# Optimization experiments

Measured on AMD Instinct MI355X. Metric: run time of the kernel, lower is better.

The kernel has to match this reference:

```python
import jax, jax.numpy as jnp
import numpy as np

N = 50000      # nodes
E = 800000     # edges
F_IN = 128     # num_features
H = 64         # hidden_dim
G = 64         # graphs in batch
EPS = 1e-5


def setup_inputs() -> dict:
    ks = jax.random.split(jax.random.key(0), 16)
    x = jax.random.normal(ks[0], (N, F_IN), dtype=jnp.float32)
    edge_index = jax.random.randint(ks[1], (2, E), 0, N, dtype=jnp.int64)
    batch = jnp.sort(jax.random.randint(ks[2], (N,), 0, G, dtype=jnp.int64))
    s = 0.05
    inp = {"x": x, "edge_index": edge_index, "batch": batch}
    # GCNConv layers: W [out,in], bias [out]; BatchNorm gamma/beta [H]
    dims = [(H, F_IN), (H, H), (H, H)]
    for i, (o, ci) in enumerate(dims):
        inp[f"W{i}"] = jax.random.normal(ks[3 + i], (o, ci), dtype=jnp.float32) * s
        inp[f"b{i}"] = jnp.zeros((o,), dtype=jnp.float32)
        inp[f"g{i}"] = jnp.ones((o,), dtype=jnp.float32)
        inp[f"be{i}"] = jnp.zeros((o,), dtype=jnp.float32)
    inp["lin1_w"] = jax.random.normal(ks[10], (H // 2, H), dtype=jnp.float32) * s
    inp["lin1_b"] = jnp.zeros((H // 2,), dtype=jnp.float32)
    inp["lin2_w"] = jax.random.normal(ks[11], (1, H // 2), dtype=jnp.float32) * s
    inp["lin2_b"] = jnp.zeros((1,), dtype=jnp.float32)
    return inp


def _gcn_conv(x, src, dst, W, b):
    # PyG GCNConv: h = x W^T; add self-loops; symmetric deg^{-1/2} norm; scatter-add; + bias
    h = x @ W.T                                   # [N, out]
    n = x.shape[0]
    deg = jax.ops.segment_sum(jnp.ones(src.shape[0], h.dtype), dst, num_segments=n) + 1.0
    dinv = jax.lax.rsqrt(deg)                     # [N]
    msg = h[src] * (dinv[src] * dinv[dst])[:, None]   # per-edge messages
    agg = jax.ops.segment_sum(msg, dst, num_segments=n)
    agg = agg + h * (dinv * dinv)[:, None]        # self-loop contribution
    return agg + b


def _bn_relu(x, g, be):
    # BatchNorm1d (training-mode batch stats, biased var) + ReLU; dropout = identity (eval)
    m = x.mean(axis=0)
    v = jnp.var(x, axis=0)
    return jax.nn.relu((x - m) * jax.lax.rsqrt(v + EPS) * g + be)


def reference(x, edge_index, batch,
              W0, b0, g0, be0, W1, b1, g1, be1, W2, b2, g2, be2,
              lin1_w, lin1_b, lin2_w, lin2_b):
    src, dst = edge_index[0], edge_index[1]
    Ws = [(W0, b0, g0, be0), (W1, b1, g1, be1), (W2, b2, g2, be2)]
    h = x
    for (W, b, g, be) in Ws:
        h = _bn_relu(_gcn_conv(h, src, dst, W, b), g, be)
    # global mean pool over graphs
    sums = jax.ops.segment_sum(h, batch, num_segments=G)          # [G, H]
    cnt = jax.ops.segment_sum(jnp.ones((h.shape[0],), h.dtype), batch, num_segments=G)
    pooled = sums / jnp.maximum(cnt, 1.0)[:, None]
    h = jax.nn.relu(pooled @ lin1_w.T + lin1_b)
    return h @ lin2_w.T + lin2_b                                   # [G, 1]
```

## Files before the change

### kernel.cpp

```cpp
#include <hip/hip_runtime.h>

#define NN 50000
#define NE 800000
#define FIN 128
#define H 64
#define NG 64
#define BN_EPS 1e-5f
#define INV_N (1.0f / 50000.0f)
#define NB_SCAN 196
#define NBKT 196

__global__ void deg_count(const int* __restrict__ dst, int* __restrict__ deg, int E) {
    int e = blockIdx.x * blockDim.x + threadIdx.x;
    if (e < E) atomicAdd(&deg[dst[e]], 1);
}

__global__ void setup_misc(const int* __restrict__ deg, float* __restrict__ dinv,
                           const float* __restrict__ W0, const float* __restrict__ W1,
                           const float* __restrict__ W2, float* __restrict__ Wt0,
                           float* __restrict__ Wt1, float* __restrict__ Wt2,
                           float* __restrict__ sl0, float* __restrict__ sl1,
                           float* __restrict__ sl2, float* __restrict__ poolcnt, int n) {
    int i = blockIdx.x * 256 + threadIdx.x;
    if (i < n) dinv[i] = rsqrtf((float)deg[i] + 1.0f);
    if (i < 64 * 128) { sl0[i] = 0.f; sl1[i] = 0.f; sl2[i] = 0.f; }
    if (i < NG * H + NG) poolcnt[i] = 0.f;
    if (i < FIN * 64) {
        int k = i >> 6, o = i & 63;
        Wt0[i] = W0[o * FIN + k];
    }
    if (i < H * 64) {
        int k = i >> 6, o = i & 63;
        Wt1[i] = W1[o * H + k];
        Wt2[i] = W2[o * H + k];
    }
}

__global__ void scan_block(const int* __restrict__ deg, int* __restrict__ row_start,
                           int* __restrict__ aux, int n) {
    __shared__ int s[256];
    int i = blockIdx.x * 256 + threadIdx.x;
    int v = (i < n) ? deg[i] : 0;
    s[threadIdx.x] = v;
    __syncthreads();
    for (int off = 1; off < 256; off <<= 1) {
        int t = (threadIdx.x >= off) ? s[threadIdx.x - off] : 0;
        __syncthreads();
        s[threadIdx.x] += t;
        __syncthreads();
    }
    if (i < n) row_start[i] = s[threadIdx.x] - v;
    if (threadIdx.x == 255) aux[blockIdx.x] = s[255];
}

__global__ void scan_aux(int* __restrict__ aux, int nb) {
    __shared__ int s[256];
    int v = (threadIdx.x < nb) ? aux[threadIdx.x] : 0;
    s[threadIdx.x] = v;
    __syncthreads();
    for (int off = 1; off < 256; off <<= 1) {
        int t = (threadIdx.x >= off) ? s[threadIdx.x - off] : 0;
        __syncthreads();
        s[threadIdx.x] += t;
        __syncthreads();
    }
    if (threadIdx.x < nb) aux[threadIdx.x] = s[threadIdx.x] - v;
}

__global__ void scan_fixup(int* __restrict__ row_start, const int* __restrict__ aux,
                           int* __restrict__ bb, int* __restrict__ bcur, int n, int E) {
    int i = blockIdx.x * 256 + threadIdx.x;
    if (i < n) {
        int rs = row_start[i] + aux[i >> 8];
        row_start[i] = rs;
        if ((i & 255) == 0) { bb[i >> 8] = rs; bcur[i >> 8] = rs; }
    }
    if (i == 0) { row_start[n] = E; bb[NBKT] = E; }
}

__global__ void bin_edges(const int* __restrict__ src, const int* __restrict__ dst,
                          int* __restrict__ bcur, unsigned int* __restrict__ staged, int E) {
    __shared__ int cnt[NBKT];
    __shared__ int offs[NBKT];
    const int chunk = (E + gridDim.x - 1) / gridDim.x;
    const int e0 = blockIdx.x * chunk;
    const int e1 = min(e0 + chunk, E);
    for (int i = threadIdx.x; i < NBKT; i += 256) cnt[i] = 0;
    __syncthreads();
    for (int e = e0 + threadIdx.x; e < e1; e += 256) atomicAdd(&cnt[dst[e] >> 8], 1);
    __syncthreads();
    for (int i = threadIdx.x; i < NBKT; i += 256) {
        int c = cnt[i];
        offs[i] = c ? atomicAdd(&bcur[i], c) : 0;
        cnt[i] = 0;
    }
    __syncthreads();
    for (int e = e0 + threadIdx.x; e < e1; e += 256) {
        int d = dst[e];
        int bkt = d >> 8;
        int idx = atomicAdd(&cnt[bkt], 1);
        staged[offs[bkt] + idx] = (unsigned int)src[e] | ((unsigned int)(d & 255) << 16);
    }
}

__global__ void csr_build(const unsigned int* __restrict__ staged,
                          const int* __restrict__ row_start, const int* __restrict__ bb,
                          int* __restrict__ csr_src, int n) {
    __shared__ int cur[256];
    int b = blockIdx.x;
    int node = b * 256 + threadIdx.x;
    cur[threadIdx.x] = (node < n) ? row_start[node] : 0;
    __syncthreads();
    int e0 = bb[b], e1 = bb[b + 1];
    for (int e = e0 + threadIdx.x; e < e1; e += 256) {
        unsigned int u = staged[e];
        int j = atomicAdd(&cur[(u >> 16) & 255], 1);
        csr_src[j] = (int)(u & 0xFFFFu);
    }
}

template <int K>
__global__ __launch_bounds__(256, 4) void matmul_tile(const float* __restrict__ x,
                                                      const float* __restrict__ Wtg,
                                                      const float* __restrict__ st,
                                                      const float* __restrict__ gamma,
                                                      const float* __restrict__ beta,
                                                      float* __restrict__ out, int n) {
    __shared__ float Xs[64 * 68];
    __shared__ float Ws[64 * 64];
    const int base = blockIdx.x * 64;
    const int q = threadIdx.x >> 4;
    const int co = (threadIdx.x & 15) * 4;

    float4 a0 = make_float4(0.f, 0.f, 0.f, 0.f);
    float4 a1 = a0, a2 = a0, a3 = a0;

    for (int kc = 0; kc < K; kc += 64) {
        if (kc) __syncthreads();
        for (int i = threadIdx.x; i < 64 * 64; i += 256) Ws[i] = Wtg[kc * 64 + i];
        {
            const int kq = (threadIdx.x & 15) * 4;
            float4 sc = make_float4(1.f, 1.f, 1.f, 1.f);
            float4 sh = make_float4(0.f, 0.f, 0.f, 0.f);
            if (st) {
                int kk = kc + kq;
                float4 s = *(const float4*)&st[kk];
                float4 ss = *(const float4*)&st[64 + kk];
                float4 gm = *(const float4*)&gamma[kk];
                float4 bt = *(const float4*)&beta[kk];
                float mx = s.x * INV_N, my = s.y * INV_N, mz = s.z * INV_N, mw = s.w * INV_N;
                sc.x = gm.x * rsqrtf(ss.x * INV_N - mx * mx + BN_EPS);
                sc.y = gm.y * rsqrtf(ss.y * INV_N - my * my + BN_EPS);
                sc.z = gm.z * rsqrtf(ss.z * INV_N - mz * mz + BN_EPS);
                sc.w = gm.w * rsqrtf(ss.w * INV_N - mw * mw + BN_EPS);
                sh.x = bt.x - mx * sc.x;
                sh.y = bt.y - my * sc.y;
                sh.z = bt.z - mz * sc.z;
                sh.w = bt.w - mw * sc.w;
            }
            for (int j = 0; j < 4; ++j) {
                int r = (threadIdx.x >> 4) + j * 16;
                int row = base + r;
                float4 v = make_float4(0.f, 0.f, 0.f, 0.f);
                if (row < n) v = *(const float4*)&x[(size_t)row * K + kc + kq];
                if (st) {
                    v.x = fmaxf(v.x * sc.x + sh.x, 0.f);
                    v.y = fmaxf(v.y * sc.y + sh.y, 0.f);
                    v.z = fmaxf(v.z * sc.z + sh.z, 0.f);
                    v.w = fmaxf(v.w * sc.w + sh.w, 0.f);
                }
                *(float4*)&Xs[r * 68 + kq] = v;
            }
        }
        __syncthreads();

#pragma unroll 2
        for (int k = 0; k < 64; k += 4) {
            float4 x0 = *(const float4*)&Xs[(q + 0) * 68 + k];
            float4 x1 = *(const float4*)&Xs[(q + 16) * 68 + k];
            float4 x2 = *(const float4*)&Xs[(q + 32) * 68 + k];
            float4 x3 = *(const float4*)&Xs[(q + 48) * 68 + k];
            float4 w0 = *(const float4*)&Ws[(k + 0) * 64 + co];
            float4 w1 = *(const float4*)&Ws[(k + 1) * 64 + co];
            float4 w2 = *(const float4*)&Ws[(k + 2) * 64 + co];
            float4 w3 = *(const float4*)&Ws[(k + 3) * 64 + co];

            a0.x += x0.x * w0.x + x0.y * w1.x + x0.z * w2.x + x0.w * w3.x;
            a0.y += x0.x * w0.y + x0.y * w1.y + x0.z * w2.y + x0.w * w3.y;
            a0.z += x0.x * w0.z + x0.y * w1.z + x0.z * w2.z + x0.w * w3.z;
            a0.w += x0.x * w0.w + x0.y * w1.w + x0.z * w2.w + x0.w * w3.w;

            a1.x += x1.x * w0.x + x1.y * w1.x + x1.z * w2.x + x1.w * w3.x;
            a1.y += x1.x * w0.y + x1.y * w1.y + x1.z * w2.y + x1.w * w3.y;
            a1.z += x1.x * w0.z + x1.y * w1.z + x1.z * w2.z + x1.w * w3.z;
            a1.w += x1.x * w0.w + x1.y * w1.w + x1.z * w2.w + x1.w * w3.w;

            a2.x += x2.x * w0.x + x2.y * w1.x + x2.z * w2.x + x2.w * w3.x;
            a2.y += x2.x * w0.y + x2.y * w1.y + x2.z * w2.y + x2.w * w3.y;
            a2.z += x2.x * w0.z + x2.y * w1.z + x2.z * w2.z + x2.w * w3.z;
            a2.w += x2.x * w0.w + x2.y * w1.w + x2.z * w2.w + x2.w * w3.w;

            a3.x += x3.x * w0.x + x3.y * w1.x + x3.z * w2.x + x3.w * w3.x;
            a3.y += x3.x * w0.y + x3.y * w1.y + x3.z * w2.y + x3.w * w3.y;
            a3.z += x3.x * w0.z + x3.y * w1.z + x3.z * w2.z + x3.w * w3.z;
            a3.w += x3.x * w0.w + x3.y * w1.w + x3.z * w2.w + x3.w * w3.w;
        }
    }

    int r0 = base + q;
    if (r0 < n) *(float4*)&out[(size_t)r0 * H + co] = a0;
    if (r0 + 16 < n) *(float4*)&out[(size_t)(r0 + 16) * H + co] = a1;
    if (r0 + 32 < n) *(float4*)&out[(size_t)(r0 + 32) * H + co] = a2;
    if (r0 + 48 < n) *(float4*)&out[(size_t)(r0 + 48) * H + co] = a3;
}

__global__ void gcn_gather(const float* __restrict__ h, const int* __restrict__ row_start,
                           const int* __restrict__ csr_src, const float* __restrict__ dinv,
                           const float* __restrict__ bias, float* __restrict__ out,
                           float* __restrict__ slots, int n) {
    const int wv = threadIdx.x >> 6;
    const int c = threadIdx.x & 63;
    const int d0 = blockIdx.x * 8 + wv * 2;
    float vA = 0.f, vB = 0.f;
    if (d0 < n) {
        const int d1 = d0 + 1;
        int jA = row_start[d0];
        const int jm = row_start[d1];
        const int je = row_start[d1 + 1];
        int jB = jm;
        float diA = dinv[d0], diB = dinv[d1];
        float bA = h[(size_t)d0 * H + c] * diA * diA + bias[c];
        float bB = h[(size_t)d1 * H + c] * diB * diB + bias[c];
        float a0 = 0.f, a1 = 0.f, a2 = 0.f, a3 = 0.f;
        float b0 = 0.f, b1 = 0.f, b2 = 0.f, b3 = 0.f;
        while (jA + 4 <= jm && jB + 4 <= je) {
            int sA0 = csr_src[jA + 0], sA1 = csr_src[jA + 1];
            int sA2 = csr_src[jA + 2], sA3 = csr_src[jA + 3];
            int sB0 = csr_src[jB + 0], sB1 = csr_src[jB + 1];
            int sB2 = csr_src[jB + 2], sB3 = csr_src[jB + 3];
            float wA0 = dinv[sA0], wA1 = dinv[sA1], wA2 = dinv[sA2], wA3 = dinv[sA3];
            float wB0 = dinv[sB0], wB1 = dinv[sB1], wB2 = dinv[sB2], wB3 = dinv[sB3];
            a0 += h[(size_t)sA0 * H + c] * wA0;
            a1 += h[(size_t)sA1 * H + c] * wA1;
            a2 += h[(size_t)sA2 * H + c] * wA2;
            a3 += h[(size_t)sA3 * H + c] * wA3;
            b0 += h[(size_t)sB0 * H + c] * wB0;
            b1 += h[(size_t)sB1 * H + c] * wB1;
            b2 += h[(size_t)sB2 * H + c] * wB2;
            b3 += h[(size_t)sB3 * H + c] * wB3;
            jA += 4;
            jB += 4;
        }
        for (; jA + 4 <= jm; jA += 4) {
            int s0 = csr_src[jA + 0], s1 = csr_src[jA + 1];
            int s2 = csr_src[jA + 2], s3 = csr_src[jA + 3];
            float w0 = dinv[s0], w1 = dinv[s1], w2 = dinv[s2], w3 = dinv[s3];
            a0 += h[(size_t)s0 * H + c] * w0;
            a1 += h[(size_t)s1 * H + c] * w1;
            a2 += h[(size_t)s2 * H + c] * w2;
            a3 += h[(size_t)s3 * H + c] * w3;
        }
        for (; jA < jm; ++jA) {
            int s = csr_src[jA];
            a0 += h[(size_t)s * H + c] * dinv[s];
        }
        for (; jB + 4 <= je; jB += 4) {
            int s0 = csr_src[jB + 0], s1 = csr_src[jB + 1];
            int s2 = csr_src[jB + 2], s3 = csr_src[jB + 3];
            float w0 = dinv[s0], w1 = dinv[s1], w2 = dinv[s2], w3 = dinv[s3];
            b0 += h[(size_t)s0 * H + c] * w0;
            b1 += h[(size_t)s1 * H + c] * w1;
            b2 += h[(size_t)s2 * H + c] * w2;
            b3 += h[(size_t)s3 * H + c] * w3;
        }
        for (; jB < je; ++jB) {
            int s = csr_src[jB];
            b0 += h[(size_t)s * H + c] * dinv[s];
        }
        vA = bA + diA * ((a0 + a1) + (a2 + a3));
        vB = bB + diB * ((b0 + b1) + (b2 + b3));
        out[(size_t)d0 * H + c] = vA;
        out[(size_t)d1 * H + c] = vB;
    }
    __shared__ float ls[256], lq[256];
    ls[threadIdx.x] = vA + vB;
    lq[threadIdx.x] = vA * vA + vB * vB;
    __syncthreads();
    if (wv == 0) {
        float s = ls[c] + ls[c + 64] + ls[c + 128] + ls[c + 192];
        float q = lq[c] + lq[c + 64] + lq[c + 128] + lq[c + 192];
        float* slot = slots + (blockIdx.x & 63) * 128;
        atomicAdd(&slot[c], s);
        atomicAdd(&slot[64 + c], q);
    }
}

__global__ void reduce_slots(const float* __restrict__ slots, float* __restrict__ st) {
    int c = threadIdx.x;
    float s0 = 0.f, s1 = 0.f, s2 = 0.f, s3 = 0.f;
    for (int k = 0; k < 64; k += 4) {
        s0 += slots[(k + 0) * 128 + c];
        s1 += slots[(k + 1) * 128 + c];
        s2 += slots[(k + 2) * 128 + c];
        s3 += slots[(k + 3) * 128 + c];
    }
    st[c] = (s0 + s1) + (s2 + s3);
}

#define PROWS 16
__global__ void pool_seg(const float* __restrict__ h, const float* __restrict__ st,
                         const float* __restrict__ gamma, const float* __restrict__ beta,
                         const int* __restrict__ batch, float* __restrict__ pool,
                         float* __restrict__ cnt, int n) {
    int wave = blockIdx.x * 4 + (threadIdx.x >> 6);
    int c = threadIdx.x & 63;
    int r0 = wave * PROWS;
    if (r0 >= n) return;
    int r1 = min(r0 + PROWS, n);
    float mean = st[c] * INV_N;
    float var = st[64 + c] * INV_N - mean * mean;
    float sc = gamma[c] * rsqrtf(var + BN_EPS);
    float sh = beta[c] - mean * sc;
    int cur = batch[r0];
    float acc = 0.f;
    int nlocal = 0;
    for (int r = r0; r < r1; ++r) {
        int g = batch[r];
        if (g != cur) {
            atomicAdd(&pool[cur * H + c], acc);
            if (c == 0) atomicAdd(&cnt[cur], (float)nlocal);
            cur = g;
            acc = 0.f;
            nlocal = 0;
        }
        acc += fmaxf(h[(size_t)r * H + c] * sc + sh, 0.f);
        ++nlocal;
    }
    atomicAdd(&pool[cur * H + c], acc);
    if (c == 0) atomicAdd(&cnt[cur], (float)nlocal);
}

__global__ void final_mlp(const float* __restrict__ pool, const float* __restrict__ cnt,
                          const float* __restrict__ l1w, const float* __restrict__ l1b,
                          const float* __restrict__ l2w, const float* __restrict__ l2b,
                          float* __restrict__ out) {
    int tid = blockIdx.x * 256 + threadIdx.x;
    int g = tid >> 5;
    int j = tid & 31;
    if (g >= NG) return;
    float inv = 1.0f / fmaxf(cnt[g], 1.0f);
    float s = l1b[j];
    for (int k = 0; k < H; ++k) s += pool[g * H + k] * inv * l1w[j * H + k];
    float v = fmaxf(s, 0.0f) * l2w[j];
    for (int off = 16; off > 0; off >>= 1) v += __shfl_down(v, off, 32);
    if (j == 0) out[g] = v + l2b[0];
}

extern "C" void kernel_launch(void* const* d_in, const int* in_sizes, int n_in,
                              void* d_out, int out_size, void* d_ws, size_t ws_size,
                              hipStream_t stream) {
    const float* x = (const float*)d_in[0];
    const int* ei = (const int*)d_in[1];
    const int* batch = (const int*)d_in[2];
    const float* W[3] = {(const float*)d_in[3], (const float*)d_in[7], (const float*)d_in[11]};
    const float* b[3] = {(const float*)d_in[4], (const float*)d_in[8], (const float*)d_in[12]};
    const float* g[3] = {(const float*)d_in[5], (const float*)d_in[9], (const float*)d_in[13]};
    const float* be[3] = {(const float*)d_in[6], (const float*)d_in[10], (const float*)d_in[14]};
    const float* l1w = (const float*)d_in[15];
    const float* l1b = (const float*)d_in[16];
    const float* l2w = (const float*)d_in[17];
    const float* l2b = (const float*)d_in[18];
    float* out = (float*)d_out;

    const int* src = ei;
    const int* dst = ei + NE;

    char* wsb = (char*)d_ws;
    size_t off = 0;
    auto alloc = [&](size_t elems) {
        void* p = wsb + off;
        off += elems * 4;
        return p;
    };
    float* dinv = (float*)alloc(50048);
    float* bufA = (float*)alloc((size_t)NN * H);
    float* bufB = (float*)alloc((size_t)NN * H);
    float* slots[3] = {(float*)alloc(64 * 128), (float*)alloc(64 * 128), (float*)alloc(64 * 128)};
    float* st[3] = {(float*)alloc(128), (float*)alloc(128), (float*)alloc(128)};
    float* pool = (float*)alloc(NG * H);
    float* cnt = (float*)alloc(64);
    float* Wt[3] = {(float*)alloc(FIN * 64), (float*)alloc(H * 64), (float*)alloc(H * 64)};
    int* deg = (int*)alloc(50048);
    int* row_start = (int*)alloc(50112);
    int* aux = (int*)alloc(256);
    int* bb = (int*)alloc(256);
    int* bcur = (int*)alloc(256);
    unsigned int* staged = (unsigned int*)alloc(NE);
    int* csr_src = (int*)alloc(NE);

    hipMemsetAsync(deg, 0, NN * sizeof(int), stream);
    deg_count<<<(NE + 255) / 256, 256, 0, stream>>>(dst, deg, NE);
    setup_misc<<<NB_SCAN, 256, 0, stream>>>(deg, dinv, W[0], W[1], W[2], Wt[0], Wt[1], Wt[2],
                                            slots[0], slots[1], slots[2], pool, NN);
    scan_block<<<NB_SCAN, 256, 0, stream>>>(deg, row_start, aux, NN);
    scan_aux<<<1, 256, 0, stream>>>(aux, NB_SCAN);
    scan_fixup<<<NB_SCAN, 256, 0, stream>>>(row_start, aux, bb, bcur, NN, NE);
    bin_edges<<<256, 256, 0, stream>>>(src, dst, bcur, staged, NE);
    csr_build<<<NBKT, 256, 0, stream>>>(staged, row_start, bb, csr_src, NN);

    const int grid_mm = (NN + 63) / 64;
    const int grid_gather = (NN + 7) / 8;

    for (int L = 0; L < 3; ++L) {
        if (L == 0)
            matmul_tile<FIN><<<grid_mm, 256, 0, stream>>>(x, Wt[0], nullptr, nullptr, nullptr,
                                                          bufA, NN);
        else
            matmul_tile<H><<<grid_mm, 256, 0, stream>>>(bufB, Wt[L], st[L - 1], g[L - 1],
                                                        be[L - 1], bufA, NN);
        gcn_gather<<<grid_gather, 256, 0, stream>>>(bufA, row_start, csr_src, dinv, b[L], bufB,
                                                    slots[L], NN);
        reduce_slots<<<1, 128, 0, stream>>>(slots[L], st[L]);
    }

    const int pool_waves = (NN + PROWS - 1) / PROWS;
    pool_seg<<<(pool_waves + 3) / 4, 256, 0, stream>>>(bufB, st[2], g[2], be[2], batch, pool,
                                                       cnt, NN);
    final_mlp<<<8, 256, 0, stream>>>(pool, cnt, l1w, l1b, l2w, l2b, out);
}
```

Measured before the change: 377.7 us.

## Build CSR via bucket histogram and per-bucket local scan, dropping global degree pass

Replaces the global per-node degree atomics, the memset and the three-kernel scan with a per-bucket histogram and a single-block bucket scan. Per-node degrees, row_start and dinv are now computed inside csr_build with a shared-memory count and scan over each bucket's staged edges. This removes 800K global atomics and several launches. In exchange, csr_build reads its staged edges twice.

After: 344.7 us. 1.1x faster.

```diff
diff --git a/kernel.cpp b/kernel.cpp
--- a/kernel.cpp
+++ b/kernel.cpp
@@ -7,24 +7,18 @@
 #define NG 64
 #define BN_EPS 1e-5f
 #define INV_N (1.0f / 50000.0f)
-#define NB_SCAN 196
 #define NBKT 196
 
-__global__ void deg_count(const int* __restrict__ dst, int* __restrict__ deg, int E) {
-    int e = blockIdx.x * blockDim.x + threadIdx.x;
-    if (e < E) atomicAdd(&deg[dst[e]], 1);
-}
-
-__global__ void setup_misc(const int* __restrict__ deg, float* __restrict__ dinv,
-                           const float* __restrict__ W0, const float* __restrict__ W1,
+__global__ void setup_misc(const float* __restrict__ W0, const float* __restrict__ W1,
                            const float* __restrict__ W2, float* __restrict__ Wt0,
                            float* __restrict__ Wt1, float* __restrict__ Wt2,
                            float* __restrict__ sl0, float* __restrict__ sl1,
-                           float* __restrict__ sl2, float* __restrict__ poolcnt, int n) {
+                           float* __restrict__ sl2, float* __restrict__ poolcnt,
+                           int* __restrict__ bktcnt) {
     int i = blockIdx.x * 256 + threadIdx.x;
-    if (i < n) dinv[i] = rsqrtf((float)deg[i] + 1.0f);
     if (i < 64 * 128) { sl0[i] = 0.f; sl1[i] = 0.f; sl2[i] = 0.f; }
     if (i < NG * H + NG) poolcnt[i] = 0.f;
+    if (i < NBKT) bktcnt[i] = 0;
     if (i < FIN * 64) {
         int k = i >> 6, o = i & 63;
         Wt0[i] = W0[o * FIN + k];
@@ -36,11 +30,23 @@
     }
 }
 
-__global__ void scan_block(const int* __restrict__ deg, int* __restrict__ row_start,
-                           int* __restrict__ aux, int n) {
+__global__ void bucket_hist(const int* __restrict__ dst, int* __restrict__ bktcnt, int E) {
+    __shared__ int cnt[NBKT];
+    const int chunk = (E + gridDim.x - 1) / gridDim.x;
+    const int e0 = blockIdx.x * chunk;
+    const int e1 = min(e0 + chunk, E);
+    for (int i = threadIdx.x; i < NBKT; i += 256) cnt[i] = 0;
+    __syncthreads();
+    for (int e = e0 + threadIdx.x; e < e1; e += 256) atomicAdd(&cnt[dst[e] >> 8], 1);
+    __syncthreads();
+    for (int i = threadIdx.x; i < NBKT; i += 256)
+        if (cnt[i]) atomicAdd(&bktcnt[i], cnt[i]);
+}
+
+__global__ void bucket_scan(const int* __restrict__ bktcnt, int* __restrict__ bb,
+                            int* __restrict__ bcur, int E) {
     __shared__ int s[256];
-    int i = blockIdx.x * 256 + threadIdx.x;
-    int v = (i < n) ? deg[i] : 0;
+    int v = (threadIdx.x < NBKT) ? bktcnt[threadIdx.x] : 0;
     s[threadIdx.x] = v;
     __syncthreads();
     for (int off = 1; off < 256; off <<= 1) {
@@ -49,33 +55,12 @@
         s[threadIdx.x] += t;
         __syncthreads();
     }
-    if (i < n) row_start[i] = s[threadIdx.x] - v;
-    if (threadIdx.x == 255) aux[blockIdx.x] = s[255];
-}
-
-__global__ void scan_aux(int* __restrict__ aux, int nb) {
-    __shared__ int s[256];
-    int v = (threadIdx.x < nb) ? aux[threadIdx.x] : 0;
-    s[threadIdx.x] = v;
-    __syncthreads();
-    for (int off = 1; off < 256; off <<= 1) {
-        int t = (threadIdx.x >= off) ? s[threadIdx.x - off] : 0;
-        __syncthreads();
-        s[threadIdx.x] += t;
-        __syncthreads();
-    }
-    if (threadIdx.x < nb) aux[threadIdx.x] = s[threadIdx.x] - v;
-}
-
-__global__ void scan_fixup(int* __restrict__ row_start, const int* __restrict__ aux,
-                           int* __restrict__ bb, int* __restrict__ bcur, int n, int E) {
-    int i = blockIdx.x * 256 + threadIdx.x;
-    if (i < n) {
-        int rs = row_start[i] + aux[i >> 8];
-        row_start[i] = rs;
-        if ((i & 255) == 0) { bb[i >> 8] = rs; bcur[i >> 8] = rs; }
-    }
-    if (i == 0) { row_start[n] = E; bb[NBKT] = E; }
+    if (threadIdx.x < NBKT) {
+        int base = s[threadIdx.x] - v;
+        bb[threadIdx.x] = base;
+        bcur[threadIdx.x] = base;
+    }
+    if (threadIdx.x == 0) bb[NBKT] = E;
 }
 
 __global__ void bin_edges(const int* __restrict__ src, const int* __restrict__ dst,
@@ -103,15 +88,37 @@
     }
 }
 
-__global__ void csr_build(const unsigned int* __restrict__ staged,
-                          const int* __restrict__ row_start, const int* __restrict__ bb,
-                          int* __restrict__ csr_src, int n) {
+__global__ void csr_build(const unsigned int* __restrict__ staged, const int* __restrict__ bb,
+                          int* __restrict__ row_start, float* __restrict__ dinv,
+                          int* __restrict__ csr_src, int n, int E) {
+    __shared__ int cnt[256];
+    __shared__ int loc[256];
     __shared__ int cur[256];
-    int b = blockIdx.x;
-    int node = b * 256 + threadIdx.x;
-    cur[threadIdx.x] = (node < n) ? row_start[node] : 0;
-    __syncthreads();
-    int e0 = bb[b], e1 = bb[b + 1];
+    const int b = blockIdx.x;
+    cnt[threadIdx.x] = 0;
+    __syncthreads();
+    const int e0 = bb[b], e1 = bb[b + 1];
+    for (int e = e0 + threadIdx.x; e < e1; e += 256)
+        atomicAdd(&cnt[(staged[e] >> 16) & 255], 1);
+    __syncthreads();
+    int v = cnt[threadIdx.x];
+    loc[threadIdx.x] = v;
+    __syncthreads();
+    for (int off = 1; off < 256; off <<= 1) {
+        int t = (threadIdx.x >= off) ? loc[threadIdx.x - off] : 0;
+        __syncthreads();
+        loc[threadIdx.x] += t;
+        __syncthreads();
+    }
+    const int start = e0 + loc[threadIdx.x] - v;
+    const int node = b * 256 + threadIdx.x;
+    if (node < n) {
+        row_start[node] = start;
+        dinv[node] = rsqrtf((float)v + 1.0f);
+    }
+    if (node == n) row_start[n] = E;
+    cur[threadIdx.x] = start;
+    __syncthreads();
     for (int e = e0 + threadIdx.x; e < e1; e += 256) {
         unsigned int u = staged[e];
         int j = atomicAdd(&cur[(u >> 16) & 255], 1);
@@ -390,23 +397,19 @@
     float* pool = (float*)alloc(NG * H);
     float* cnt = (float*)alloc(64);
     float* Wt[3] = {(float*)alloc(FIN * 64), (float*)alloc(H * 64), (float*)alloc(H * 64)};
-    int* deg = (int*)alloc(50048);
     int* row_start = (int*)alloc(50112);
-    int* aux = (int*)alloc(256);
+    int* bktcnt = (int*)alloc(256);
     int* bb = (int*)alloc(256);
     int* bcur = (int*)alloc(256);
     unsigned int* staged = (unsigned int*)alloc(NE);
     int* csr_src = (int*)alloc(NE);
 
-    hipMemsetAsync(deg, 0, NN * sizeof(int), stream);
-    deg_count<<<(NE + 255) / 256, 256, 0, stream>>>(dst, deg, NE);
-    setup_misc<<<NB_SCAN, 256, 0, stream>>>(deg, dinv, W[0], W[1], W[2], Wt[0], Wt[1], Wt[2],
-                                            slots[0], slots[1], slots[2], pool, NN);
-    scan_block<<<NB_SCAN, 256, 0, stream>>>(deg, row_start, aux, NN);
-    scan_aux<<<1, 256, 0, stream>>>(aux, NB_SCAN);
-    scan_fixup<<<NB_SCAN, 256, 0, stream>>>(row_start, aux, bb, bcur, NN, NE);
+    setup_misc<<<32, 256, 0, stream>>>(W[0], W[1], W[2], Wt[0], Wt[1], Wt[2], slots[0], slots[1],
+                                       slots[2], pool, bktcnt);
+    bucket_hist<<<256, 256, 0, stream>>>(dst, bktcnt, NE);
+    bucket_scan<<<1, 256, 0, stream>>>(bktcnt, bb, bcur, NE);
     bin_edges<<<256, 256, 0, stream>>>(src, dst, bcur, staged, NE);
-    csr_build<<<NBKT, 256, 0, stream>>>(staged, row_start, bb, csr_src, NN);
+    csr_build<<<NBKT, 256, 0, stream>>>(staged, bb, row_start, dinv, csr_src, NN, NE);
 
     const int grid_mm = (NN + 63) / 64;
     const int grid_gather = (NN + 7) / 8;
```
